# Kernel tuning notes

Hardware: AMD Instinct MI355X
Metric: run time of the kernel (lower is better)

The kernel has to match this reference:

```python
import jax, jax.numpy as jnp
import numpy as np

ALPHA = 0.25
GAMMA = 2.0


def setup_inputs() -> dict:
    key = jax.random.key(0)
    k1, k2, k3, k4, k5, k6, k7, k8 = jax.random.split(key, 8)
    B, A, C, M = 8, 120000, 80, 32
    # sigmoid-ed class probabilities in (0,1)
    classifications = jax.random.uniform(k1, (B, A, C), jnp.float32, 1e-4, 1.0 - 1e-4)
    regressions = jax.random.normal(k2, (B, A, 4), jnp.float32) * 0.1
    # anchors in [y1, x1, y2, x2] (widths = a[:,3]-a[:,1] in original code)
    cx = jax.random.uniform(k3, (A,), jnp.float32, 0.0, 800.0)
    cy = jax.random.uniform(k4, (A,), jnp.float32, 0.0, 800.0)
    wh = jax.random.uniform(k5, (A, 2), jnp.float32, 16.0, 256.0)  # (w, h)
    anchors = jnp.stack([cy - 0.5 * wh[:, 1], cx - 0.5 * wh[:, 0],
                         cy + 0.5 * wh[:, 1], cx + 0.5 * wh[:, 0]], axis=1)[None]  # [1,A,4]
    # annotations per image: [x1, y1, x2, y2, class]
    xy1 = jax.random.uniform(k6, (B, M, 2), jnp.float32, 0.0, 600.0)
    bwh = jax.random.uniform(k7, (B, M, 2), jnp.float32, 20.0, 200.0)
    cls_ids = jax.random.randint(k8, (B, M, 1), 0, C).astype(jnp.float32)
    annotations = jnp.concatenate([xy1, xy1 + bwh, cls_ids], axis=2)
    return dict(classifications=classifications, regressions=regressions,
                anchors=anchors, annotations=annotations)


def _calc_iou(a, b):
    # a: anchors [A,4] in [y1,x1,y2,x2]; b: gt boxes [M,4] in [x1,y1,x2,y2]
    m = jnp.max(a)
    a = a / m
    b = b / m
    area = (b[:, 2] - b[:, 0]) * (b[:, 3] - b[:, 1])                 # [M]
    iw = jnp.minimum(a[:, 3:4], b[:, 2]) - jnp.maximum(a[:, 1:2], b[:, 0])  # [A,M]
    ih = jnp.minimum(a[:, 2:3], b[:, 3]) - jnp.maximum(a[:, 0:1], b[:, 1])
    iw = jnp.maximum(iw, 0.0)
    ih = jnp.maximum(ih, 0.0)
    ua = ((a[:, 2] - a[:, 0]) * (a[:, 3] - a[:, 1]))[:, None] + area - iw * ih
    ua = jnp.maximum(ua, 1e-8)
    return iw * ih / ua                                              # [A,M]


def _giou_loss(pred, gt):
    # pred, gt: [A,4] in [x1,y1,x2,y2]
    px1 = jnp.minimum(pred[:, 0], pred[:, 2]); py1 = jnp.minimum(pred[:, 1], pred[:, 3])
    px2 = jnp.maximum(pred[:, 0], pred[:, 2]); py2 = jnp.maximum(pred[:, 1], pred[:, 3])
    gx1 = jnp.minimum(gt[:, 0], gt[:, 2]);     gy1 = jnp.minimum(gt[:, 1], gt[:, 3])
    gx2 = jnp.maximum(gt[:, 0], gt[:, 2]);     gy2 = jnp.maximum(gt[:, 1], gt[:, 3])
    iw = jnp.maximum(jnp.minimum(px2, gx2) - jnp.maximum(px1, gx1), 0.0)
    ih = jnp.maximum(jnp.minimum(py2, gy2) - jnp.maximum(py1, gy1), 0.0)
    inter = iw * ih
    area_p = jnp.maximum((px2 - px1) * (py2 - py1), 1e-6)
    area_g = jnp.maximum((gx2 - gx1) * (gy2 - gy1), 1e-6)
    union = area_p + area_g - inter
    iou = inter / (union + 1e-7)
    wc = jnp.maximum(jnp.maximum(px2, gx2) - jnp.minimum(px1, gx1), 1e-6)
    hc = jnp.maximum(jnp.maximum(py2, gy2) - jnp.minimum(py1, gy1), 1e-6)
    area_c = wc * hc
    giou = jnp.clip(iou - (area_c - union) / (area_c + 1e-7), -1.0, 1.0)
    return 1.0 - giou


def _reorder(b):
    return jnp.stack([jnp.minimum(b[:, 0], b[:, 2]), jnp.minimum(b[:, 1], b[:, 3]),
                      jnp.maximum(b[:, 0], b[:, 2]), jnp.maximum(b[:, 1], b[:, 3])], axis=1)


def reference(classifications, regressions, anchors, annotations):
    anchor = anchors[0]                                   # [A,4] (y1,x1,y2,x2)
    aw = anchor[:, 3] - anchor[:, 1]
    ah = anchor[:, 2] - anchor[:, 0]
    acx = anchor[:, 1] + 0.5 * aw
    acy = anchor[:, 0] + 0.5 * ah
    C = classifications.shape[-1]

    def per_image(cls, reg, ann):
        cls = jnp.clip(cls, 0.0005, 1.0 - 0.0005)          # [A,C]
        iou = _calc_iou(anchor, ann[:, :4])                # [A,M]
        iou_max = jnp.max(iou, axis=1)
        iou_arg = jnp.argmax(iou, axis=1)
        assigned = ann[iou_arg]                            # [A,5]
        pos = iou_max >= 0.5                               # [A]
        t = jnp.full_like(cls, -1.0)
        t = jnp.where((iou_max < 0.4)[:, None], 0.0, t)
        onehot = jax.nn.one_hot(assigned[:, 4].astype(jnp.int32), C, dtype=cls.dtype)
        t = jnp.where(pos[:, None], onehot, t)
        alpha_factor = jnp.where(t == 1.0, ALPHA, 1.0 - ALPHA)
        focal_w = alpha_factor * jnp.where(t == 1.0, 1.0 - cls, cls) ** GAMMA
        bce = -(t * jnp.log(cls) + (1.0 - t) * jnp.log(1.0 - cls))
        cls_loss = jnp.where(t != -1.0, focal_w * bce, 0.0)
        npos = jnp.sum(pos).astype(cls.dtype)
        c_loss = jnp.sum(cls_loss) / jnp.maximum(npos, 1.0)
        # decode predicted boxes for ALL anchors (mask positives in the reduction)
        ty, tx, th, tw = reg[:, 0], reg[:, 1], reg[:, 2], reg[:, 3]
        pcx = tx * aw + acx
        pcy = ty * ah + acy
        pw = jnp.exp(tw) * aw
        ph = jnp.exp(th) * ah
        pred = jnp.stack([pcx - 0.5 * pw, pcy - 0.5 * ph,
                          pcx + 0.5 * pw, pcy + 0.5 * ph], axis=1)
        pred = jnp.maximum(pred, 0.0)
        gt = jnp.maximum(assigned[:, :4], 0.0)
        giou = _giou_loss(_reorder(pred), _reorder(gt))    # [A]
        r_loss = jnp.where(npos > 0,
                           jnp.sum(giou * pos.astype(cls.dtype)) / jnp.maximum(npos, 1.0),
                           0.0)
        return c_loss, r_loss

    c, r = jax.vmap(per_image)(classifications, regressions, annotations)
    c_loss = jnp.mean(c)
    r_loss = jnp.mean(r)
    return c_loss + r_loss, c_loss, r_loss
```

## Files before the change

### kernel.cpp

```cpp
#include <hip/hip_runtime.h>

#define B_IMG 8
#define A_TOTAL 120000
#define C_CLS 80
#define M_ANN 32
#define APB 256
#define THREADS 256
#define NBLK_X 469
#define NBLK   (NBLK_X * B_IMG)
#define NEG075LN2 (-0.51986038542f)

__global__ __launch_bounds__(THREADS) void focal_main_kernel(
    const float* __restrict__ cls,
    const float* __restrict__ reg,
    const float* __restrict__ anchors,
    const float* __restrict__ ann,
    float* __restrict__ ws)
{
    __shared__ float m_s[APB];
    __shared__ float red_c[4], red_r[4], red_n[4];

    const int b   = blockIdx.y;
    const int a0  = blockIdx.x * APB;
    const int tid = threadIdx.x;
    const int nA  = min(APB, A_TOTAL - a0);
    const float* __restrict__ annb = ann + b * (M_ANN * 5);

    float r_acc = 0.0f, n_acc = 0.0f, c_acc = 0.0f;
    float mval  = 0.0f;

    if (tid < nA) {
        const int a = a0 + tid;
        float4 anc = ((const float4*)anchors)[a];
        float ay1 = anc.x, ax1 = anc.y, ay2 = anc.z, ax2 = anc.w;
        float area_a = (ay2 - ay1) * (ax2 - ax1);
        float binter = 0.0f, bua = 1.0f;
        int   barg = 0;
        #pragma unroll
        for (int j = 0; j < M_ANN; ++j) {
            float bx1 = annb[j * 5 + 0], by1 = annb[j * 5 + 1];
            float bx2 = annb[j * 5 + 2], by2 = annb[j * 5 + 3];
            float iw = fmaxf(fminf(ax2, bx2) - fmaxf(ax1, bx1), 0.0f);
            float ih = fmaxf(fminf(ay2, by2) - fmaxf(ay1, by1), 0.0f);
            float inter = iw * ih;
            float ua = fmaxf(area_a + (bx2 - bx1) * (by2 - by1) - inter, 1e-8f);
            bool gt = inter * bua > binter * ua;
            binter = gt ? inter : binter;
            bua    = gt ? ua    : bua;
            barg   = gt ? j     : barg;
        }
        bool pos = binter >= 0.5f * bua;
        bool neg = binter <  0.4f * bua;
        mval = (pos || neg) ? NEG075LN2 : 0.0f;

        if (pos) {
            n_acc = 1.0f;
            int k = (int)annb[barg * 5 + 4];
            float cv = cls[((size_t)b * A_TOTAL + a) * C_CLS + k];
            float c  = fminf(fmaxf(cv, 5e-4f), 1.0f - 5e-4f);
            float omc = 1.0f - c;
            c_acc += 0.25f * omc * omc * (-__logf(c))
                   - 0.75f * c * c * (-__logf(omc));

            float4 rg = ((const float4*)reg)[(size_t)b * A_TOTAL + a];
            float ty = rg.x, tx = rg.y, th = rg.z, tw = rg.w;
            float aw = ax2 - ax1, ah = ay2 - ay1;
            float acx = ax1 + 0.5f * aw, acy = ay1 + 0.5f * ah;
            float pcx = tx * aw + acx, pcy = ty * ah + acy;
            float pw = __expf(tw) * aw, ph = __expf(th) * ah;
            float px1 = fmaxf(pcx - 0.5f * pw, 0.0f);
            float py1 = fmaxf(pcy - 0.5f * ph, 0.0f);
            float px2 = fmaxf(pcx + 0.5f * pw, 0.0f);
            float py2 = fmaxf(pcy + 0.5f * ph, 0.0f);
            float gx1 = fmaxf(annb[barg * 5 + 0], 0.0f);
            float gy1 = fmaxf(annb[barg * 5 + 1], 0.0f);
            float gx2 = fmaxf(annb[barg * 5 + 2], 0.0f);
            float gy2 = fmaxf(annb[barg * 5 + 3], 0.0f);
            float iw2 = fmaxf(fminf(px2, gx2) - fmaxf(px1, gx1), 0.0f);
            float ih2 = fmaxf(fminf(py2, gy2) - fmaxf(py1, gy1), 0.0f);
            float inter2 = iw2 * ih2;
            float area_p = fmaxf((px2 - px1) * (py2 - py1), 1e-6f);
            float area_g = fmaxf((gx2 - gx1) * (gy2 - gy1), 1e-6f);
            float uni = area_p + area_g - inter2;
            float iou2 = inter2 / (uni + 1e-7f);
            float wc = fmaxf(fmaxf(px2, gx2) - fminf(px1, gx1), 1e-6f);
            float hc = fmaxf(fmaxf(py2, gy2) - fminf(py1, gy1), 1e-6f);
            float area_c = wc * hc;
            float giou = fminf(fmaxf(iou2 - (area_c - uni) / (area_c + 1e-7f), -1.0f), 1.0f);
            r_acc = 1.0f - giou;
        }
    }
    m_s[tid] = (tid < nA) ? mval : 0.0f;
    __syncthreads();

    const float4* __restrict__ cp =
        (const float4*)(cls + ((size_t)b * A_TOTAL + a0) * C_CLS);

#define FOCAL4(v, idx)                                                    \
    {                                                                     \
        float m_ = m_s[(unsigned)(idx) / 20u];                            \
        float s_, c_;                                                     \
        c_ = fminf(fmaxf((v).x, 5e-4f), 1.0f - 5e-4f);                    \
        s_ = c_ * c_ * __log2f(1.0f - c_);                                \
        c_ = fminf(fmaxf((v).y, 5e-4f), 1.0f - 5e-4f);                    \
        s_ = fmaf(c_ * c_, __log2f(1.0f - c_), s_);                       \
        c_ = fminf(fmaxf((v).z, 5e-4f), 1.0f - 5e-4f);                    \
        s_ = fmaf(c_ * c_, __log2f(1.0f - c_), s_);                       \
        c_ = fminf(fmaxf((v).w, 5e-4f), 1.0f - 5e-4f);                    \
        s_ = fmaf(c_ * c_, __log2f(1.0f - c_), s_);                       \
        c_acc = fmaf(m_, s_, c_acc);                                      \
    }

    if (nA == APB) {
        #pragma unroll
        for (int g = 0; g < 2; ++g) {
            const int base = tid + g * 2560;
            float4 v0 = cp[base];
            float4 v1 = cp[base + 256];
            float4 v2 = cp[base + 512];
            float4 v3 = cp[base + 768];
            float4 v4 = cp[base + 1024];
            float4 v5 = cp[base + 1280];
            float4 v6 = cp[base + 1536];
            float4 v7 = cp[base + 1792];
            float4 v8 = cp[base + 2048];
            float4 v9 = cp[base + 2304];
            FOCAL4(v0, base)
            FOCAL4(v1, base + 256)
            FOCAL4(v2, base + 512)
            FOCAL4(v3, base + 768)
            FOCAL4(v4, base + 1024)
            FOCAL4(v5, base + 1280)
            FOCAL4(v6, base + 1536)
            FOCAL4(v7, base + 1792)
            FOCAL4(v8, base + 2048)
            FOCAL4(v9, base + 2304)
        }
    } else {
        const int nf4 = nA * (C_CLS / 4);
        for (int i = tid; i < nf4; i += THREADS) {
            float4 v = cp[i];
            FOCAL4(v, i)
        }
    }
#undef FOCAL4

    #pragma unroll
    for (int o = 32; o > 0; o >>= 1) {
        c_acc += __shfl_down(c_acc, o);
        r_acc += __shfl_down(r_acc, o);
        n_acc += __shfl_down(n_acc, o);
    }
    int wid = tid >> 6;
    if ((tid & 63) == 0) { red_c[wid] = c_acc; red_r[wid] = r_acc; red_n[wid] = n_acc; }
    __syncthreads();
    if (tid == 0) {
        const int slot = b * NBLK_X + blockIdx.x;
        ws[slot]            = red_c[0] + red_c[1] + red_c[2] + red_c[3];
        ws[NBLK + slot]     = red_r[0] + red_r[1] + red_r[2] + red_r[3];
        ws[2 * NBLK + slot] = red_n[0] + red_n[1] + red_n[2] + red_n[3];
    }
}

__global__ __launch_bounds__(THREADS) void finalize_kernel(
    const float* __restrict__ ws, float* __restrict__ out)
{
    __shared__ float red[4][3];
    const int tid = threadIdx.x;
    float c_tot = 0.0f, r_tot = 0.0f;

    for (int b = 0; b < B_IMG; ++b) {
        float pc = 0.0f, pr = 0.0f, pn = 0.0f;
        for (int i = tid; i < NBLK_X; i += THREADS) {
            const int slot = b * NBLK_X + i;
            pc += ws[slot];
            pr += ws[NBLK + slot];
            pn += ws[2 * NBLK + slot];
        }
        #pragma unroll
        for (int o = 32; o > 0; o >>= 1) {
            pc += __shfl_down(pc, o);
            pr += __shfl_down(pr, o);
            pn += __shfl_down(pn, o);
        }
        if ((tid & 63) == 0) {
            int wid = tid >> 6;
            red[wid][0] = pc; red[wid][1] = pr; red[wid][2] = pn;
        }
        __syncthreads();
        if (tid == 0) {
            float cs = red[0][0] + red[1][0] + red[2][0] + red[3][0];
            float rs = red[0][1] + red[1][1] + red[2][1] + red[3][1];
            float ns = red[0][2] + red[1][2] + red[2][2] + red[3][2];
            c_tot += cs / fmaxf(ns, 1.0f);
            r_tot += (ns > 0.0f) ? (rs / fmaxf(ns, 1.0f)) : 0.0f;
        }
        __syncthreads();
    }
    if (tid == 0) {
        c_tot *= (1.0f / B_IMG);
        r_tot *= (1.0f / B_IMG);
        out[0] = c_tot + r_tot;
        out[1] = c_tot;
        out[2] = r_tot;
    }
}

extern "C" void kernel_launch(void* const* d_in, const int* in_sizes, int n_in,
                              void* d_out, int out_size, void* d_ws, size_t ws_size,
                              hipStream_t stream) {
    const float* cls     = (const float*)d_in[0];
    const float* reg     = (const float*)d_in[1];
    const float* anchors = (const float*)d_in[2];
    const float* ann     = (const float*)d_in[3];
    float* ws  = (float*)d_ws;
    float* out = (float*)d_out;

    dim3 grid(NBLK_X, B_IMG);
    hipLaunchKernelGGL(focal_main_kernel, grid, dim3(THREADS), 0, stream,
                       cls, reg, anchors, ann, ws);
    hipLaunchKernelGGL(finalize_kernel, dim3(1), dim3(THREADS), 0, stream, ws, out);
}
```

Before: 69.83 us.

## Split anchor assignment and focal streaming into separate kernels via workspace mask

The fused kernel becomes two. An assignment kernel does the IoU matching and the positive-anchor losses and writes a per-anchor mask weight to workspace. A streaming kernel then reads those weights and runs the bandwidth-bound focal sum over the classification tensor. The aim is to take the serial 32-box IoU loop off the front of each streaming block so its loads are not held up, at the price of an extra launch and an extra mask round trip through global memory. The finalize kernel is also rewritten to reduce all images in parallel, with one 32-lane group per image, instead of looping over them.

```diff
diff --git a/kernel.cpp b/kernel.cpp
--- a/kernel.cpp
+++ b/kernel.cpp
@@ -10,14 +10,15 @@
 #define NBLK   (NBLK_X * B_IMG)
 #define NEG075LN2 (-0.51986038542f)
 
-__global__ __launch_bounds__(THREADS) void focal_main_kernel(
+#define WS_M_OFF 16384
+
+__global__ __launch_bounds__(THREADS) void assign_kernel(
     const float* __restrict__ cls,
     const float* __restrict__ reg,
     const float* __restrict__ anchors,
     const float* __restrict__ ann,
     float* __restrict__ ws)
 {
-    __shared__ float m_s[APB];
     __shared__ float red_c[4], red_r[4], red_n[4];
 
     const int b   = blockIdx.y;
@@ -27,7 +28,6 @@
     const float* __restrict__ annb = ann + b * (M_ANN * 5);
 
     float r_acc = 0.0f, n_acc = 0.0f, c_acc = 0.0f;
-    float mval  = 0.0f;
 
     if (tid < nA) {
         const int a = a0 + tid;
@@ -51,7 +51,8 @@
         }
         bool pos = binter >= 0.5f * bua;
         bool neg = binter <  0.4f * bua;
-        mval = (pos || neg) ? NEG075LN2 : 0.0f;
+        float mval = (pos || neg) ? NEG075LN2 : 0.0f;
+        ws[WS_M_OFF + (size_t)b * A_TOTAL + a] = mval;
 
         if (pos) {
             n_acc = 1.0f;
@@ -90,11 +91,44 @@
             r_acc = 1.0f - giou;
         }
     }
-    m_s[tid] = (tid < nA) ? mval : 0.0f;
+
+    #pragma unroll
+    for (int o = 32; o > 0; o >>= 1) {
+        c_acc += __shfl_down(c_acc, o);
+        r_acc += __shfl_down(r_acc, o);
+        n_acc += __shfl_down(n_acc, o);
+    }
+    int wid = tid >> 6;
+    if ((tid & 63) == 0) { red_c[wid] = c_acc; red_r[wid] = r_acc; red_n[wid] = n_acc; }
+    __syncthreads();
+    if (tid == 0) {
+        const int slot = b * NBLK_X + blockIdx.x;
+        ws[slot]            = red_c[0] + red_c[1] + red_c[2] + red_c[3];
+        ws[NBLK + slot]     = red_r[0] + red_r[1] + red_r[2] + red_r[3];
+        ws[2 * NBLK + slot] = red_n[0] + red_n[1] + red_n[2] + red_n[3];
+    }
+}
+
+__global__ __launch_bounds__(THREADS) void focal_stream_kernel(
+    const float* __restrict__ cls,
+    const float* __restrict__ mg,
+    float* __restrict__ ws)
+{
+    __shared__ float m_s[APB];
+    __shared__ float red_c[4];
+
+    const int b   = blockIdx.y;
+    const int a0  = blockIdx.x * APB;
+    const int tid = threadIdx.x;
+    const int nA  = min(APB, A_TOTAL - a0);
+    const bool full = (nA == APB);
+
+    m_s[tid] = (tid < nA) ? mg[(size_t)b * A_TOTAL + a0 + tid] : 0.0f;
     __syncthreads();
 
     const float4* __restrict__ cp =
         (const float4*)(cls + ((size_t)b * A_TOTAL + a0) * C_CLS);
+    float c_acc = 0.0f;
 
 #define FOCAL4(v, idx)                                                    \
     {                                                                     \
@@ -111,7 +145,7 @@
         c_acc = fmaf(m_, s_, c_acc);                                      \
     }
 
-    if (nA == APB) {
+    if (full) {
         #pragma unroll
         for (int g = 0; g < 2; ++g) {
             const int base = tid + g * 2560;
@@ -146,58 +180,47 @@
 #undef FOCAL4
 
     #pragma unroll
-    for (int o = 32; o > 0; o >>= 1) {
-        c_acc += __shfl_down(c_acc, o);
-        r_acc += __shfl_down(r_acc, o);
-        n_acc += __shfl_down(n_acc, o);
-    }
+    for (int o = 32; o > 0; o >>= 1) c_acc += __shfl_down(c_acc, o);
     int wid = tid >> 6;
-    if ((tid & 63) == 0) { red_c[wid] = c_acc; red_r[wid] = r_acc; red_n[wid] = n_acc; }
+    if ((tid & 63) == 0) red_c[wid] = c_acc;
     __syncthreads();
     if (tid == 0) {
         const int slot = b * NBLK_X + blockIdx.x;
-        ws[slot]            = red_c[0] + red_c[1] + red_c[2] + red_c[3];
-        ws[NBLK + slot]     = red_r[0] + red_r[1] + red_r[2] + red_r[3];
-        ws[2 * NBLK + slot] = red_n[0] + red_n[1] + red_n[2] + red_n[3];
+        ws[3 * NBLK + slot] = red_c[0] + red_c[1] + red_c[2] + red_c[3];
     }
 }
 
 __global__ __launch_bounds__(THREADS) void finalize_kernel(
     const float* __restrict__ ws, float* __restrict__ out)
 {
-    __shared__ float red[4][3];
-    const int tid = threadIdx.x;
-    float c_tot = 0.0f, r_tot = 0.0f;
-
-    for (int b = 0; b < B_IMG; ++b) {
-        float pc = 0.0f, pr = 0.0f, pn = 0.0f;
-        for (int i = tid; i < NBLK_X; i += THREADS) {
-            const int slot = b * NBLK_X + i;
-            pc += ws[slot];
-            pr += ws[NBLK + slot];
-            pn += ws[2 * NBLK + slot];
-        }
+    __shared__ float sc[B_IMG], sr[B_IMG], sn[B_IMG];
+    const int tid    = threadIdx.x;
+    const int img    = tid >> 5;
+    const int lane32 = tid & 31;
+
+    float pc = 0.0f, pr = 0.0f, pn = 0.0f;
+    for (int i = lane32; i < NBLK_X; i += 32) {
+        const int slot = img * NBLK_X + i;
+        pc += ws[slot] + ws[3 * NBLK + slot];
+        pr += ws[NBLK + slot];
+        pn += ws[2 * NBLK + slot];
+    }
+    #pragma unroll
+    for (int o = 16; o > 0; o >>= 1) {
+        pc += __shfl_down(pc, o, 32);
+        pr += __shfl_down(pr, o, 32);
+        pn += __shfl_down(pn, o, 32);
+    }
+    if (lane32 == 0) { sc[img] = pc; sr[img] = pr; sn[img] = pn; }
+    __syncthreads();
+    if (tid == 0) {
+        float c_tot = 0.0f, r_tot = 0.0f;
         #pragma unroll
-        for (int o = 32; o > 0; o >>= 1) {
-            pc += __shfl_down(pc, o);
-            pr += __shfl_down(pr, o);
-            pn += __shfl_down(pn, o);
-        }
-        if ((tid & 63) == 0) {
-            int wid = tid >> 6;
-            red[wid][0] = pc; red[wid][1] = pr; red[wid][2] = pn;
-        }
-        __syncthreads();
-        if (tid == 0) {
-            float cs = red[0][0] + red[1][0] + red[2][0] + red[3][0];
-            float rs = red[0][1] + red[1][1] + red[2][1] + red[3][1];
-            float ns = red[0][2] + red[1][2] + red[2][2] + red[3][2];
-            c_tot += cs / fmaxf(ns, 1.0f);
-            r_tot += (ns > 0.0f) ? (rs / fmaxf(ns, 1.0f)) : 0.0f;
-        }
-        __syncthreads();
-    }
-    if (tid == 0) {
+        for (int b = 0; b < B_IMG; ++b) {
+            float ns = sn[b];
+            c_tot += sc[b] / fmaxf(ns, 1.0f);
+            r_tot += (ns > 0.0f) ? (sr[b] / fmaxf(ns, 1.0f)) : 0.0f;
+        }
         c_tot *= (1.0f / B_IMG);
         r_tot *= (1.0f / B_IMG);
         out[0] = c_tot + r_tot;
@@ -217,7 +240,9 @@
     float* out = (float*)d_out;
 
     dim3 grid(NBLK_X, B_IMG);
-    hipLaunchKernelGGL(focal_main_kernel, grid, dim3(THREADS), 0, stream,
+    hipLaunchKernelGGL(assign_kernel, grid, dim3(THREADS), 0, stream,
                        cls, reg, anchors, ann, ws);
+    hipLaunchKernelGGL(focal_stream_kernel, grid, dim3(THREADS), 0, stream,
+                       cls, ws + WS_M_OFF, ws);
     hipLaunchKernelGGL(finalize_kernel, dim3(1), dim3(THREADS), 0, stream, ws, out);
 }
```

After: 83.82 us. +20.0%, slower.
